# Kernel tuning notes

Measured on AMD Instinct MI355X. Metric: run time of the kernel, lower is better.

## Reference

```python
import jax, jax.numpy as jnp
import numpy as np

B, S, D, H = 4, 2048, 1024, 16
DH = D // H  # 64
NEG = -1e9


def setup_inputs() -> dict:
    key = jax.random.key(0)
    k1, k2, k3 = jax.random.split(key, 3)
    x = jax.random.normal(k1, (B, S, D), dtype=jnp.float32)
    w_attn = jax.random.normal(k2, (D, 3 * D), dtype=jnp.float32) * 0.02
    b_attn = jnp.zeros((3 * D,), dtype=jnp.float32)
    w_proj = jax.random.normal(k3, (D, D), dtype=jnp.float32) * 0.02
    b_proj = jnp.zeros((D,), dtype=jnp.float32)
    return {"x": x, "w_attn": w_attn, "b_attn": b_attn, "w_proj": w_proj, "b_proj": b_proj}


def reference(x, w_attn, b_attn, w_proj, b_proj):
    # c_attn: fused QKV projection (Conv1D with rf=1 == dense layer)
    qkv = x @ w_attn + b_attn  # [B,S,3D]
    q, k, v = jnp.split(qkv, 3, axis=-1)

    def split_heads(t):  # [B,S,D] -> [B,H,S,DH]
        return t.reshape(B, S, H, DH).transpose(0, 2, 1, 3)

    q, k, v = split_heads(q), split_heads(k), split_heads(v)

    # scaled scores with additive causal mask (as w*b + -1e9*(1-b))
    w = jnp.einsum("bhqd,bhkd->bhqk", q, k) / jnp.sqrt(jnp.float32(DH))
    causal = jnp.tril(jnp.ones((S, S), dtype=w.dtype))[None, None]
    w = w * causal + NEG * (1.0 - causal)
    w = jax.nn.softmax(w, axis=-1)
    # attn_dropout / resid_dropout: p=0 (eval) -> identity

    a = jnp.einsum("bhqk,bhkd->bhqd", w, v)  # [B,H,S,DH]
    a = a.transpose(0, 2, 1, 3).reshape(B, S, D)  # merge heads
    return a @ w_proj + b_proj
```

## Files before the change

### kernel.cpp

```cpp
#include <hip/hip_runtime.h>


typedef short  s8v   __attribute__((ext_vector_type(8)));
typedef float  f32x4 __attribute__((ext_vector_type(4)));
typedef float  f32x16 __attribute__((ext_vector_type(16)));
typedef unsigned short u16;
typedef u16    u16x4 __attribute__((ext_vector_type(4)));
typedef unsigned int u32;
typedef u32    u32x2 __attribute__((ext_vector_type(2)));

__device__ __forceinline__ u16 f2b(float f) {
  union { float f; unsigned u; } v; v.f = f;
  unsigned r = v.u + 0x7FFFu + ((v.u >> 16) & 1u);
  return (u16)(r >> 16);
}
__device__ __forceinline__ u32 cvtpk(float lo, float hi) {
  u32 r; asm("v_cvt_pk_bf16_f32 %0, %1, %2" : "=v"(r) : "v"(lo), "v"(hi)); return r;
}
__device__ __forceinline__ void plswap(u32 &d, u32 &s) {
  asm volatile("v_permlane32_swap_b32 %0, %1" : "+v"(d), "+v"(s));
}
__device__ __forceinline__ void gll16(const void* g, void* l) {
  __builtin_amdgcn_global_load_lds((const __attribute__((address_space(1))) void*)g,
                                   (__attribute__((address_space(3))) void*)l, 16, 0, 0);
}

#define QSCALE 0.18033688011112042f

__global__ __launch_bounds__(256) void k_cvt(const float* __restrict__ in,
                                             u16* __restrict__ out, int n4) {
  int t = blockIdx.x * 256 + threadIdx.x;
  if (t < n4) {
    f32x4 f = ((const f32x4*)in)[t];
    u16x4 o;
    o[0] = f2b(f[0]); o[1] = f2b(f[1]); o[2] = f2b(f[2]); o[3] = f2b(f[3]);
    ((u16x4*)out)[t] = o;
  }
}

__global__ __launch_bounds__(256) void k_tr(const float* __restrict__ in,
                                            u16* __restrict__ out, int R, int C) {
  __shared__ float tile[32][33];
  int c0 = blockIdx.x * 32, r0 = blockIdx.y * 32;
  int tx = threadIdx.x, ty = threadIdx.y;
#pragma unroll
  for (int j = 0; j < 4; j++)
    tile[ty + j * 8][tx] = in[(size_t)(r0 + ty + j * 8) * C + c0 + tx];
  __syncthreads();
#pragma unroll
  for (int j = 0; j < 4; j++)
    out[(size_t)(c0 + ty + j * 8) * R + r0 + tx] = f2b(tile[tx][ty + j * 8]);
}

__device__ __forceinline__ void gemm_tile(const u16* bA, const u16* bB,
                                          f32x4 (&acc)[4][4],
                                          int wr, int wc, int lr, int lg) {
  s8v af[4], bfr[4];
#pragma unroll
  for (int m = 0; m < 4; m++) {
    const int row = wr + m * 16 + lr;
    af[m] = *(const s8v*)&bA[row * 32 + (lg ^ ((row >> 1) & 3)) * 8];
  }
#pragma unroll
  for (int n = 0; n < 4; n++) {
    const int row = wc + n * 16 + lr;
    bfr[n] = *(const s8v*)&bB[row * 32 + (lg ^ ((row >> 1) & 3)) * 8];
  }
  __builtin_amdgcn_s_setprio(1);
#pragma unroll
  for (int m = 0; m < 4; m++)
#pragma unroll
    for (int n = 0; n < 4; n++)
      acc[m][n] = __builtin_amdgcn_mfma_f32_16x16x32_bf16(af[m], bfr[n], acc[m][n], 0, 0, 0);
  __builtin_amdgcn_s_setprio(0);
}

template <int EPI>
__global__ __launch_bounds__(256, 3) void k_gemm(
    const u16* __restrict__ A, const u16* __restrict__ Bt,
    const float* __restrict__ bias,
    u16* __restrict__ qb, u16* __restrict__ kb, u16* __restrict__ vb,
    float* __restrict__ outf, int M, int N, int K) {
  __shared__ u16 lA[3][4096];
  __shared__ u16 lB[3][4096];
  const int tid = threadIdx.x;
  const int lane = tid & 63, w = tid >> 6;
  const int wr = (w >> 1) * 64, wc = (w & 1) * 64;
  const int lr = lane & 15, lg = lane >> 4;

  const int nwg = gridDim.x * gridDim.y;
  const int bid = blockIdx.y * gridDim.x + blockIdx.x;
  const int swz = (bid & 7) * (nwg >> 3) + (bid >> 3);
  const int m0 = (swz / gridDim.x) * 128, n0 = (swz % gridDim.x) * 128;

  const int rr = lane >> 2;
  const int cb = ((lane & 3) ^ ((lane >> 3) & 3)) * 16;
  const size_t K2 = (size_t)K * 2;
  const char* gAc = (const char*)A + (size_t)m0 * K2;
  const char* gBc = (const char*)Bt + (size_t)n0 * K2;

  auto stage = [&](int kt, int buf) {
    const size_t ko = (size_t)kt * 64 + cb;
    char* dA = (char*)&lA[buf][0];
    char* dB = (char*)&lB[buf][0];
    gll16(gAc + (size_t)(32 * w + rr) * K2 + ko,      dA + (2 * w) * 1024);
    gll16(gAc + (size_t)(32 * w + 16 + rr) * K2 + ko, dA + (2 * w + 1) * 1024);
    gll16(gBc + (size_t)(32 * w + rr) * K2 + ko,      dB + (2 * w) * 1024);
    gll16(gBc + (size_t)(32 * w + 16 + rr) * K2 + ko, dB + (2 * w + 1) * 1024);
  };

  f32x4 acc[4][4];
  f32x4 zz = {0.f, 0.f, 0.f, 0.f};
#pragma unroll
  for (int m = 0; m < 4; m++)
#pragma unroll
    for (int n = 0; n < 4; n++) acc[m][n] = zz;

  const int nk = K / 32;
  stage(0, 0);
  if (nk > 1) stage(1, 1);

#define STEP(T, CB, SB)                                                     \
  if ((T) < nk) {                                                           \
    if ((T) + 1 < nk) { asm volatile("s_waitcnt vmcnt(4)" ::: "memory"); }  \
    else              { asm volatile("s_waitcnt vmcnt(0)" ::: "memory"); }  \
    __builtin_amdgcn_s_barrier();                                           \
    __builtin_amdgcn_sched_barrier(0);                                      \
    if ((T) + 2 < nk) stage((T) + 2, (SB));                                 \
    gemm_tile(&lA[(CB)][0], &lB[(CB)][0], acc, wr, wc, lr, lg);             \
  }

  for (int t0 = 0; t0 < nk; t0 += 3) {
    STEP(t0,     0, 2)
    STEP(t0 + 1, 1, 0)
    STEP(t0 + 2, 2, 1)
  }
#undef STEP

#pragma unroll
  for (int m = 0; m < 4; m++) {
#pragma unroll
    for (int n = 0; n < 4; n++) {
      const int col = n0 + wc + n * 16 + lr;
      const float bb = bias[col];
      const int row0 = m0 + wr + m * 16 + 4 * lg;
      if (EPI == 0) {
        const int which = col >> 10, d = col & 1023, h = d >> 6, dh = d & 63;
        if (which == 2) {
          const int b = row0 >> 11, s = row0 & 2047;
          u16x4 ov;
#pragma unroll
          for (int r = 0; r < 4; r++) ov[r] = f2b(acc[m][n][r] + bb);
          *(u16x4*)(vb + ((size_t)((b * 16 + h) * 64 + dh)) * 2048 + s) = ov;
        } else {
          u16* dst = which == 0 ? qb : kb;
          const float sc = which == 0 ? QSCALE : 1.0f;
#pragma unroll
          for (int r = 0; r < 4; r++) {
            const int row = row0 + r;
            const int b = row >> 11, s = row & 2047;
            dst[(size_t)((b * 16 + h) * 2048 + s) * 64 + dh] = f2b((acc[m][n][r] + bb) * sc);
          }
        }
      } else {
#pragma unroll
        for (int r = 0; r < 4; r++)
          outf[(size_t)(row0 + r) * N + col] = acc[m][n][r] + bb;
      }
    }
  }
}

__global__ __launch_bounds__(256, 3) void k_attn(
    const u16* __restrict__ Q, const u16* __restrict__ K,
    const u16* __restrict__ Vt, u16* __restrict__ O) {
  __shared__ u16 lKV[2][8192];
  const int x = blockIdx.x;
  const int bh = ((x & 7) << 3) | ((x >> 3) & 7);
  const int qt = 15 - (x >> 6);
  const int tid = threadIdx.x, lane = tid & 63, w = tid >> 6;
  const int l31 = lane & 31, h = lane >> 5;
  const int qbase = qt * 128 + w * 32;
  const u16* Kb = K + (size_t)bh * 2048 * 64;
  const u16* Vb = Vt + (size_t)bh * 64 * 2048;

  const int skv = tid >> 2;
  const int ssl = (tid & 3) * 2;

  s8v kR0, kR1, vR0, vR1;
  auto pref = [&](int kv0) {
    const u16* gk = Kb + (size_t)(kv0 + skv) * 64 + ssl * 8;
    const u16* gv = Vb + (size_t)skv * 2048 + kv0 + ssl * 8;
    kR0 = *(const s8v*)gk; kR1 = *(const s8v*)(gk + 8);
    vR0 = *(const s8v*)gv; vR1 = *(const s8v*)(gv + 8);
  };
  auto stage = [&](int buf) {
    u16* base = &lKV[buf][0];
    *(s8v*)&base[(ssl * 64 + (skv ^ ssl)) * 8] = kR0;
    *(s8v*)&base[((ssl + 1) * 64 + (skv ^ (ssl + 1))) * 8] = kR1;
    *(s8v*)&base[4096 + (ssl * 64 + (skv ^ ssl)) * 8] = vR0;
    *(s8v*)&base[4096 + ((ssl + 1) * 64 + (skv ^ (ssl + 1))) * 8] = vR1;
  };

  s8v qf[4];
#pragma unroll
  for (int ks = 0; ks < 4; ks++)
    qf[ks] = *(const s8v*)(Q + (size_t)(bh * 2048 + qbase + l31) * 64 + ks * 16 + 8 * h);

  f32x16 accO0, accO1;
#pragma unroll
  for (int i = 0; i < 16; i++) { accO0[i] = 0.f; accO1[i] = 0.f; }
  float mrun = -1e30f, lrun = 0.f;

  const int ntile = 2 * qt + 2;
  pref(0); stage(0);
  if (ntile > 1) pref(64);

  for (int t = 0; t < ntile; ++t) {
    const int kv0 = t * 64;
    asm volatile("s_waitcnt lgkmcnt(0)" ::: "memory");
    __builtin_amdgcn_s_barrier();
    __builtin_amdgcn_sched_barrier(0);
    const u16* base = &lKV[t & 1][0];

    if (kv0 <= qbase + 31) {
      f32x16 st0, st1;
#pragma unroll
      for (int i = 0; i < 16; i++) { st0[i] = 0.f; st1[i] = 0.f; }
      __builtin_amdgcn_s_setprio(1);
#pragma unroll
      for (int ks = 0; ks < 4; ks++) {
        const int sl = 2 * ks + h;
        s8v a0 = *(const s8v*)&base[(sl * 64 + (l31 ^ sl)) * 8];
        s8v a1 = *(const s8v*)&base[(sl * 64 + ((32 + l31) ^ sl)) * 8];
        st0 = __builtin_amdgcn_mfma_f32_32x32x16_bf16(a0, qf[ks], st0, 0, 0, 0);
        st1 = __builtin_amdgcn_mfma_f32_32x32x16_bf16(a1, qf[ks], st1, 0, 0, 0);
      }
      __builtin_amdgcn_s_setprio(0);
      if (kv0 + 63 > qbase) {
        const int dq = qbase + l31 - kv0;
#pragma unroll
        for (int r = 0; r < 16; r++) {
          const int kl = (r & 3) + 8 * (r >> 2) + 4 * h;
          if (kl > dq) st0[r] = -1e30f;
          if (kl + 32 > dq) st1[r] = -1e30f;
        }
      }
      float mx = st0[0];
#pragma unroll
      for (int r = 1; r < 16; r++) mx = fmaxf(mx, st0[r]);
#pragma unroll
      for (int r = 0; r < 16; r++) mx = fmaxf(mx, st1[r]);
      mx = fmaxf(mx, __shfl_xor(mx, 32));
      if (!__all(mx <= mrun + 11.0f)) {
        const float mnew = fmaxf(mrun, mx);
        const float f = exp2f(mrun - mnew);
        lrun *= f;
#pragma unroll
        for (int r = 0; r < 16; r++) { accO0[r] *= f; accO1[r] *= f; }
        mrun = mnew;
      }
      float s = 0.f;
#pragma unroll
      for (int r = 0; r < 16; r++) { st0[r] = exp2f(st0[r] - mrun); s += st0[r]; }
#pragma unroll
      for (int r = 0; r < 16; r++) { st1[r] = exp2f(st1[r] - mrun); s += st1[r]; }
      s += __shfl_xor(s, 32);
      lrun += s;
      u32 W0[8], W1[8];
#pragma unroll
      for (int a = 0; a < 4; a++) {
        W0[2 * a]     = cvtpk(st0[4 * a], st0[4 * a + 1]);
        W0[2 * a + 1] = cvtpk(st0[4 * a + 2], st0[4 * a + 3]);
        W1[2 * a]     = cvtpk(st1[4 * a], st1[4 * a + 1]);
        W1[2 * a + 1] = cvtpk(st1[4 * a + 2], st1[4 * a + 3]);
      }
      __builtin_amdgcn_s_setprio(1);
#pragma unroll
      for (int ks = 0; ks < 4; ks++) {
        const int kp = ks & 1;
        u32 x0 = (ks < 2) ? W0[4 * kp]     : W1[4 * kp];
        u32 y0 = (ks < 2) ? W0[4 * kp + 2] : W1[4 * kp + 2];
        u32 x1 = (ks < 2) ? W0[4 * kp + 1] : W1[4 * kp + 1];
        u32 y1 = (ks < 2) ? W0[4 * kp + 3] : W1[4 * kp + 3];
        plswap(x0, y0);
        plswap(x1, y1);
        union { u32 u[4]; s8v v; } fb;
        fb.u[0] = x0; fb.u[1] = x1; fb.u[2] = y0; fb.u[3] = y1;
        const int sl = 2 * ks + h;
        s8v va0 = *(const s8v*)&base[4096 + (sl * 64 + (l31 ^ sl)) * 8];
        s8v va1 = *(const s8v*)&base[4096 + (sl * 64 + ((32 + l31) ^ sl)) * 8];
        accO0 = __builtin_amdgcn_mfma_f32_32x32x16_bf16(va0, fb.v, accO0, 0, 0, 0);
        accO1 = __builtin_amdgcn_mfma_f32_32x32x16_bf16(va1, fb.v, accO1, 0, 0, 0);
      }
      __builtin_amdgcn_s_setprio(0);
    }
    if (t + 1 < ntile) {
      stage((t + 1) & 1);
      if (t + 2 < ntile) pref((t + 2) * 64);
    }
  }

  const int b_ = bh >> 4, h_ = bh & 15;
  const float rinv = 1.0f / lrun;
  u16* Ob = O + (size_t)(b_ * 2048 + qbase + l31) * 1024 + h_ * 64;
#pragma unroll
  for (int a = 0; a < 4; a++) {
    u32x2 o0, o1;
    o0[0] = cvtpk(accO0[4 * a] * rinv, accO0[4 * a + 1] * rinv);
    o0[1] = cvtpk(accO0[4 * a + 2] * rinv, accO0[4 * a + 3] * rinv);
    o1[0] = cvtpk(accO1[4 * a] * rinv, accO1[4 * a + 1] * rinv);
    o1[1] = cvtpk(accO1[4 * a + 2] * rinv, accO1[4 * a + 3] * rinv);
    *(u32x2*)(Ob + 8 * a + 4 * h) = o0;
    *(u32x2*)(Ob + 32 + 8 * a + 4 * h) = o1;
  }
}

extern "C" void kernel_launch(void* const* d_in, const int* in_sizes, int n_in,
                              void* d_out, int out_size, void* d_ws, size_t ws_size,
                              hipStream_t stream) {
  const float* x      = (const float*)d_in[0];
  const float* w_attn = (const float*)d_in[1];
  const float* b_attn = (const float*)d_in[2];
  const float* w_proj = (const float*)d_in[3];
  const float* b_proj = (const float*)d_in[4];
  float* out = (float*)d_out;

  u16* ws  = (u16*)d_ws;
  u16* xb  = ws;
  u16* wTa = xb + 8388608;
  u16* wTp = wTa + 3145728;
  u16* qb  = wTp + 1048576;
  u16* kb  = qb + 8388608;
  u16* vb  = kb + 8388608;

  k_cvt<<<8192, 256, 0, stream>>>(x, xb, 2097152);
  k_tr<<<dim3(96, 32), dim3(32, 8), 0, stream>>>(w_attn, wTa, 1024, 3072);
  k_tr<<<dim3(32, 32), dim3(32, 8), 0, stream>>>(w_proj, wTp, 1024, 1024);
  k_gemm<0><<<dim3(24, 64), 256, 0, stream>>>(xb, wTa, b_attn, qb, kb, vb, nullptr, 8192, 3072, 1024);
  k_attn<<<1024, 256, 0, stream>>>(qb, kb, vb, xb);
  k_gemm<1><<<dim3(8, 64), 256, 0, stream>>>(xb, wTp, b_proj, nullptr, nullptr, nullptr, out, 8192, 1024, 1024);
}
```

Baseline: 182.6 us.

## Widen GEMM tiles to 128x256 and stage attention K/V via direct global-to-LDS loads

The GEMM kernels now compute 128x256 output tiles, with each warp owning 64x128 and 32 accumulators, and the grids are halved to match. This raises arithmetic intensity per LDS byte loaded but increases register pressure, so occupancy is lowered to 2. Separately, the attention kernel drops its register prefetch-then-store staging of K/V in favour of global_load_lds DMA into the double buffer, issued right after the barrier. The new attention wait uses vmcnt(0) each tile, which may expose load latency.

```diff
diff --git a/kernel.cpp b/kernel.cpp
--- a/kernel.cpp
+++ b/kernel.cpp
@@ -53,16 +53,16 @@
 }
 
 __device__ __forceinline__ void gemm_tile(const u16* bA, const u16* bB,
-                                          f32x4 (&acc)[4][4],
+                                          f32x4 (&acc)[4][8],
                                           int wr, int wc, int lr, int lg) {
-  s8v af[4], bfr[4];
+  s8v af[4], bfr[8];
 #pragma unroll
   for (int m = 0; m < 4; m++) {
     const int row = wr + m * 16 + lr;
     af[m] = *(const s8v*)&bA[row * 32 + (lg ^ ((row >> 1) & 3)) * 8];
   }
 #pragma unroll
-  for (int n = 0; n < 4; n++) {
+  for (int n = 0; n < 8; n++) {
     const int row = wc + n * 16 + lr;
     bfr[n] = *(const s8v*)&bB[row * 32 + (lg ^ ((row >> 1) & 3)) * 8];
   }
@@ -70,28 +70,28 @@
 #pragma unroll
   for (int m = 0; m < 4; m++)
 #pragma unroll
-    for (int n = 0; n < 4; n++)
+    for (int n = 0; n < 8; n++)
       acc[m][n] = __builtin_amdgcn_mfma_f32_16x16x32_bf16(af[m], bfr[n], acc[m][n], 0, 0, 0);
   __builtin_amdgcn_s_setprio(0);
 }
 
 template <int EPI>
-__global__ __launch_bounds__(256, 3) void k_gemm(
+__global__ __launch_bounds__(256, 2) void k_gemm(
     const u16* __restrict__ A, const u16* __restrict__ Bt,
     const float* __restrict__ bias,
     u16* __restrict__ qb, u16* __restrict__ kb, u16* __restrict__ vb,
     float* __restrict__ outf, int M, int N, int K) {
   __shared__ u16 lA[3][4096];
-  __shared__ u16 lB[3][4096];
+  __shared__ u16 lB[3][8192];
   const int tid = threadIdx.x;
   const int lane = tid & 63, w = tid >> 6;
-  const int wr = (w >> 1) * 64, wc = (w & 1) * 64;
+  const int wr = (w >> 1) * 64, wc = (w & 1) * 128;
   const int lr = lane & 15, lg = lane >> 4;
 
   const int nwg = gridDim.x * gridDim.y;
   const int bid = blockIdx.y * gridDim.x + blockIdx.x;
   const int swz = (bid & 7) * (nwg >> 3) + (bid >> 3);
-  const int m0 = (swz / gridDim.x) * 128, n0 = (swz % gridDim.x) * 128;
+  const int m0 = (swz / gridDim.x) * 128, n0 = (swz % gridDim.x) * 256;
 
   const int rr = lane >> 2;
   const int cb = ((lane & 3) ^ ((lane >> 3) & 3)) * 16;
@@ -103,18 +103,24 @@
     const size_t ko = (size_t)kt * 64 + cb;
     char* dA = (char*)&lA[buf][0];
     char* dB = (char*)&lB[buf][0];
-    gll16(gAc + (size_t)(32 * w + rr) * K2 + ko,      dA + (2 * w) * 1024);
-    gll16(gAc + (size_t)(32 * w + 16 + rr) * K2 + ko, dA + (2 * w + 1) * 1024);
-    gll16(gBc + (size_t)(32 * w + rr) * K2 + ko,      dB + (2 * w) * 1024);
-    gll16(gBc + (size_t)(32 * w + 16 + rr) * K2 + ko, dB + (2 * w + 1) * 1024);
+#pragma unroll
+    for (int i = 0; i < 2; i++) {
+      const int sg = 2 * w + i;
+      gll16(gAc + (size_t)(16 * sg + rr) * K2 + ko, dA + sg * 1024);
+    }
+#pragma unroll
+    for (int i = 0; i < 4; i++) {
+      const int sg = 4 * w + i;
+      gll16(gBc + (size_t)(16 * sg + rr) * K2 + ko, dB + sg * 1024);
+    }
   };
 
-  f32x4 acc[4][4];
+  f32x4 acc[4][8];
   f32x4 zz = {0.f, 0.f, 0.f, 0.f};
 #pragma unroll
   for (int m = 0; m < 4; m++)
 #pragma unroll
-    for (int n = 0; n < 4; n++) acc[m][n] = zz;
+    for (int n = 0; n < 8; n++) acc[m][n] = zz;
 
   const int nk = K / 32;
   stage(0, 0);
@@ -122,7 +128,7 @@
 
 #define STEP(T, CB, SB)                                                     \
   if ((T) < nk) {                                                           \
-    if ((T) + 1 < nk) { asm volatile("s_waitcnt vmcnt(4)" ::: "memory"); }  \
+    if ((T) + 1 < nk) { asm volatile("s_waitcnt vmcnt(6)" ::: "memory"); }  \
     else              { asm volatile("s_waitcnt vmcnt(0)" ::: "memory"); }  \
     __builtin_amdgcn_s_barrier();                                           \
     __builtin_amdgcn_sched_barrier(0);                                      \
@@ -140,7 +146,7 @@
 #pragma unroll
   for (int m = 0; m < 4; m++) {
 #pragma unroll
-    for (int n = 0; n < 4; n++) {
+    for (int n = 0; n < 8; n++) {
       const int col = n0 + wc + n * 16 + lr;
       const float bb = bias[col];
       const int row0 = m0 + wr + m * 16 + 4 * lg;
@@ -184,22 +190,15 @@
   const u16* Kb = K + (size_t)bh * 2048 * 64;
   const u16* Vb = Vt + (size_t)bh * 64 * 2048;
 
-  const int skv = tid >> 2;
-  const int ssl = (tid & 3) * 2;
-
-  s8v kR0, kR1, vR0, vR1;
-  auto pref = [&](int kv0) {
-    const u16* gk = Kb + (size_t)(kv0 + skv) * 64 + ssl * 8;
-    const u16* gv = Vb + (size_t)skv * 2048 + kv0 + ssl * 8;
-    kR0 = *(const s8v*)gk; kR1 = *(const s8v*)(gk + 8);
-    vR0 = *(const s8v*)gv; vR1 = *(const s8v*)(gv + 8);
-  };
-  auto stage = [&](int buf) {
-    u16* base = &lKV[buf][0];
-    *(s8v*)&base[(ssl * 64 + (skv ^ ssl)) * 8] = kR0;
-    *(s8v*)&base[((ssl + 1) * 64 + (skv ^ (ssl + 1))) * 8] = kR1;
-    *(s8v*)&base[4096 + (ssl * 64 + (skv ^ ssl)) * 8] = vR0;
-    *(s8v*)&base[4096 + ((ssl + 1) * 64 + (skv ^ (ssl + 1))) * 8] = vR1;
+  auto stage_dma = [&](int kv0, int buf) {
+    char* base = (char*)&lKV[buf][0];
+#pragma unroll
+    for (int i = 0; i < 2; i++) {
+      const int sg = 2 * w + i;
+      const int r = lane ^ sg;
+      gll16(Kb + (size_t)(kv0 + r) * 64 + sg * 8, base + sg * 1024);
+      gll16(Vb + (size_t)r * 2048 + kv0 + sg * 8, base + 8192 + sg * 1024);
+    }
   };
 
   s8v qf[4];
@@ -213,14 +212,14 @@
   float mrun = -1e30f, lrun = 0.f;
 
   const int ntile = 2 * qt + 2;
-  pref(0); stage(0);
-  if (ntile > 1) pref(64);
+  stage_dma(0, 0);
 
   for (int t = 0; t < ntile; ++t) {
     const int kv0 = t * 64;
-    asm volatile("s_waitcnt lgkmcnt(0)" ::: "memory");
+    asm volatile("s_waitcnt vmcnt(0)" ::: "memory");
     __builtin_amdgcn_s_barrier();
     __builtin_amdgcn_sched_barrier(0);
+    if (t + 1 < ntile) stage_dma((t + 1) * 64, (t + 1) & 1);
     const u16* base = &lKV[t & 1][0];
 
     if (kv0 <= qbase + 31) {
@@ -295,10 +294,6 @@
       }
       __builtin_amdgcn_s_setprio(0);
     }
-    if (t + 1 < ntile) {
-      stage((t + 1) & 1);
-      if (t + 2 < ntile) pref((t + 2) * 64);
-    }
   }
 
   const int b_ = bh >> 4, h_ = bh & 15;
@@ -337,7 +332,7 @@
   k_cvt<<<8192, 256, 0, stream>>>(x, xb, 2097152);
   k_tr<<<dim3(96, 32), dim3(32, 8), 0, stream>>>(w_attn, wTa, 1024, 3072);
   k_tr<<<dim3(32, 32), dim3(32, 8), 0, stream>>>(w_proj, wTp, 1024, 1024);
-  k_gemm<0><<<dim3(24, 64), 256, 0, stream>>>(xb, wTa, b_attn, qb, kb, vb, nullptr, 8192, 3072, 1024);
+  k_gemm<0><<<dim3(12, 64), 256, 0, stream>>>(xb, wTa, b_attn, qb, kb, vb, nullptr, 8192, 3072, 1024);
   k_attn<<<1024, 256, 0, stream>>>(qb, kb, vb, xb);
-  k_gemm<1><<<dim3(8, 64), 256, 0, stream>>>(xb, wTp, b_proj, nullptr, nullptr, nullptr, out, 8192, 1024, 1024);
-}
+  k_gemm<1><<<dim3(4, 64), 256, 0, stream>>>(xb, wTp, b_proj, nullptr, nullptr, nullptr, out, 8192, 1024, 1024);
+}
```

Result: slower. 200.7 us (+9.9%).
